# Kernel optimization log

Hardware: AMD Instinct MI355X
Metric: run time of the kernel (lower is better)

## Reference

```python
import jax, jax.numpy as jnp
import numpy as np

N_NODES = 50000
N_EDGES = 800000
IN_FEATS = 256
HIDDEN = 128
OUT_FEATS = 64


def setup_inputs() -> dict:
    key = jax.random.key(0)
    k1, k2, k3, k4, k5 = jax.random.split(key, 5)
    x = jax.random.normal(k1, (N_NODES, IN_FEATS), dtype=jnp.float32)
    src = jax.random.randint(k2, (N_EDGES,), 0, N_NODES, dtype=jnp.int64)
    dst = jax.random.randint(k3, (N_EDGES,), 0, N_NODES, dtype=jnp.int64)
    # Glorot-ish init for linear weights (DGL GraphConv uses xavier_uniform)
    W1 = jax.random.normal(k4, (IN_FEATS, HIDDEN), dtype=jnp.float32) / np.sqrt(IN_FEATS)
    W2 = jax.random.normal(k5, (HIDDEN, OUT_FEATS), dtype=jnp.float32) / np.sqrt(HIDDEN)
    b1 = jnp.zeros((HIDDEN,), dtype=jnp.float32)
    b2 = jnp.zeros((OUT_FEATS,), dtype=jnp.float32)
    return {"x": x, "src": src, "dst": dst, "W1": W1, "b1": b1, "W2": W2, "b2": b2}


def _norms(src, dst, n_nodes):
    ones = jnp.ones(src.shape[0], dtype=jnp.float32)
    deg_out = jax.ops.segment_sum(ones, src, num_segments=n_nodes)
    deg_in = jax.ops.segment_sum(ones, dst, num_segments=n_nodes)
    # DGL clamps zero degrees to 1 to avoid inf
    norm_src = jnp.power(jnp.clip(deg_out, 1.0, None), -0.5)  # [N]
    norm_dst = jnp.power(jnp.clip(deg_in, 1.0, None), -0.5)   # [N]
    return norm_src, norm_dst


def _gcn_layer(h, W, b, src, dst, norm_src, norm_dst, n_nodes):
    # norm='both': D_dst^{-1/2} A D_src^{-1/2} (h W) + b
    # multiply by W first (in_feats >= out_feats -> cheaper aggregation)
    m = (h * norm_src[:, None]) @ W            # [N, out]
    agg = jax.ops.segment_sum(m[src], dst, num_segments=n_nodes)  # [N, out]
    return agg * norm_dst[:, None] + b


def reference(x, src, dst, W1, b1, W2, b2):
    n = x.shape[0]
    norm_src, norm_dst = _norms(src, dst, n)
    h = _gcn_layer(x, W1, b1, src, dst, norm_src, norm_dst, n)
    h = jax.nn.relu(h)
    h = _gcn_layer(h, W2, b2, src, dst, norm_src, norm_dst, n)
    return h
```

## Files before the change

kernel.cpp:

```cpp
#include <hip/hip_runtime.h>

#define N_NODES 50000
#define N_EDGES 800000
#define IN_FEATS 256
#define HIDDEN 128
#define OUT_FEATS 64

#define NB 16384
#define NRANGE 4
#define NBT (NRANGE * NB)
#define NCHUNK 64
#define EPC 12500

typedef _Float16 f16;
typedef _Float16 f16x8 __attribute__((ext_vector_type(8)));
typedef float f32x4 __attribute__((ext_vector_type(4)));

__global__ __launch_bounds__(256) void hist_kernel(
    const int* __restrict__ src, const int* __restrict__ dst,
    unsigned* __restrict__ hist_src, unsigned* __restrict__ hist_dst,
    const float* __restrict__ W1, const float* __restrict__ W2,
    f16* __restrict__ W1T, f16* __restrict__ W2T) {
  __shared__ unsigned ls[NB / 2];
  __shared__ unsigned ld2[NB / 2];
  const int r = blockIdx.x % NRANGE;
  const int c = blockIdx.x / NRANGE;
  const int lo = r * NB;
  for (int i = threadIdx.x; i < NB / 2; i += 256) {
    ls[i] = 0;
    ld2[i] = 0;
  }
  __syncthreads();
  const int4* s4 = (const int4*)(src + c * EPC);
  const int4* d4 = (const int4*)(dst + c * EPC);
  for (int i = threadIdx.x; i < EPC / 4; i += 256) {
    int4 s = s4[i];
    int4 d = d4[i];
    unsigned b;
    b = (unsigned)(s.x - lo); if (b < NB) atomicAdd(&ls[b >> 1], 1u << ((b & 1) << 4));
    b = (unsigned)(s.y - lo); if (b < NB) atomicAdd(&ls[b >> 1], 1u << ((b & 1) << 4));
    b = (unsigned)(s.z - lo); if (b < NB) atomicAdd(&ls[b >> 1], 1u << ((b & 1) << 4));
    b = (unsigned)(s.w - lo); if (b < NB) atomicAdd(&ls[b >> 1], 1u << ((b & 1) << 4));
    b = (unsigned)(d.x - lo); if (b < NB) atomicAdd(&ld2[b >> 1], 1u << ((b & 1) << 4));
    b = (unsigned)(d.y - lo); if (b < NB) atomicAdd(&ld2[b >> 1], 1u << ((b & 1) << 4));
    b = (unsigned)(d.z - lo); if (b < NB) atomicAdd(&ld2[b >> 1], 1u << ((b & 1) << 4));
    b = (unsigned)(d.w - lo); if (b < NB) atomicAdd(&ld2[b >> 1], 1u << ((b & 1) << 4));
  }
  __syncthreads();
  unsigned* hs = hist_src + ((long)c * NBT + lo) / 2;
  unsigned* hd = hist_dst + ((long)c * NBT + lo) / 2;
  for (int i = threadIdx.x; i < NB / 2; i += 256) {
    hs[i] = ls[i];
    hd[i] = ld2[i];
  }
  if (blockIdx.x < 160) {
    int i = blockIdx.x * 256 + threadIdx.x;
    if (i < 128 * 256) {
      int n = i >> 8, k = i & 255;
      W1T[i] = (f16)W1[k * 128 + n];
    } else {
      int j = i - 128 * 256;
      int n = j >> 7, k = j & 127;
      W2T[j] = (f16)W2[k * 64 + n];
    }
  }
}

__global__ __launch_bounds__(256) void reduce_kernel(
    const unsigned* __restrict__ hist_src, unsigned* __restrict__ hist_dst,
    int* __restrict__ deg_in, float* __restrict__ norm_src,
    float* __restrict__ norm_dst, int* __restrict__ partial) {
  const unsigned short* hs = (const unsigned short*)hist_src;
  unsigned short* hd = (unsigned short*)hist_dst;
  int n = blockIdx.x * 256 + threadIdx.x;
  int run = 0;
  if (n < N_NODES) {
    int so = 0;
#pragma unroll 8
    for (int c = 0; c < NCHUNK; ++c) so += hs[(long)c * NBT + n];
    norm_src[n] = rsqrtf((float)max(so, 1));
#pragma unroll 8
    for (int c = 0; c < NCHUNK; ++c) {
      int t = hd[(long)c * NBT + n];
      hd[(long)c * NBT + n] = (unsigned short)run;
      run += t;
    }
    deg_in[n] = run;
    norm_dst[n] = rsqrtf((float)max(run, 1));
  }
  __shared__ int sd[256];
  sd[threadIdx.x] = run;
  __syncthreads();
  for (int s = 128; s > 0; s >>= 1) {
    if (threadIdx.x < s) sd[threadIdx.x] += sd[threadIdx.x + s];
    __syncthreads();
  }
  if (threadIdx.x == 0) partial[blockIdx.x] = sd[0];
}

__global__ __launch_bounds__(256) void scan3(const int* __restrict__ deg,
                                             const int* __restrict__ partial,
                                             int* __restrict__ rowptr) {
  __shared__ int sd[256];
  __shared__ int sp[256];
  const int w = blockIdx.x;
  int pv = (threadIdx.x < 196) ? partial[threadIdx.x] : 0;
  sp[threadIdx.x] = pv;
  __syncthreads();
  for (int off = 1; off < 256; off <<= 1) {
    int t = sp[threadIdx.x] +
            ((threadIdx.x >= off) ? sp[threadIdx.x - off] : 0);
    __syncthreads();
    sp[threadIdx.x] = t;
    __syncthreads();
  }
  const int base = (w == 0) ? 0 : sp[w - 1];
  int i = w * 256 + threadIdx.x;
  int v = (i < N_NODES) ? deg[i] : 0;
  sd[threadIdx.x] = v;
  __syncthreads();
  for (int off = 1; off < 256; off <<= 1) {
    int t = sd[threadIdx.x] +
            ((threadIdx.x >= off) ? sd[threadIdx.x - off] : 0);
    __syncthreads();
    sd[threadIdx.x] = t;
    __syncthreads();
  }
  if (i < N_NODES) rowptr[i] = base + sd[threadIdx.x] - v;
  if (w == 0 && threadIdx.x == 0) rowptr[N_NODES] = N_EDGES;
}

__global__ __launch_bounds__(256) void fill_csr(
    const int* __restrict__ src, const int* __restrict__ dst,
    const int* __restrict__ rowptr, const unsigned* __restrict__ pref32,
    int* __restrict__ col) {
  __shared__ int cur[NB];
  const unsigned short* pref = (const unsigned short*)pref32;
  const int r = blockIdx.x % NRANGE;
  const int c = blockIdx.x / NRANGE;
  const int lo = r * NB;
  for (int i = threadIdx.x; i < NB; i += 256) {
    int n = lo + i;
    cur[i] = (n < N_NODES) ? rowptr[n] + pref[(long)c * NBT + n] : 0;
  }
  __syncthreads();
  const int4* s4 = (const int4*)(src + c * EPC);
  const int4* d4 = (const int4*)(dst + c * EPC);
  for (int i = threadIdx.x; i < EPC / 4; i += 256) {
    int4 s = s4[i];
    int4 d = d4[i];
    unsigned b;
    b = (unsigned)(d.x - lo);
    if (b < NB) col[atomicAdd(&cur[b], 1)] = s.x;
    b = (unsigned)(d.y - lo);
    if (b < NB) col[atomicAdd(&cur[b], 1)] = s.y;
    b = (unsigned)(d.z - lo);
    if (b < NB) col[atomicAdd(&cur[b], 1)] = s.z;
    b = (unsigned)(d.w - lo);
    if (b < NB) col[atomicAdd(&cur[b], 1)] = s.w;
  }
}

template <int K, int NC, int TN, bool FP32IN>
__global__ __launch_bounds__(256) void gemm_mfma(
    const void* __restrict__ Xv, const f16* __restrict__ WT,
    const float* __restrict__ ns, f16* __restrict__ Mout) {
  constexpr int KI = K / 32;
  constexpr int COLBLK = NC / (TN * 16);
  constexpr int KP = K + 8;
  __shared__ f16 Bs[TN * 16 * KP];

  const int cb = blockIdx.x % COLBLK;
  const int rb = blockIdx.x / COLBLK;
  const int col0 = cb * TN * 16;
  const int wave = threadIdx.x >> 6;
  const int lane = threadIdx.x & 63;
  const int m = lane & 15;
  const int q = lane >> 4;
  const int row0 = rb * 64 + wave * 16;

  for (int idx = threadIdx.x; idx < TN * 16 * (K / 8); idx += 256) {
    int n = idx / (K / 8);
    int kk = idx % (K / 8);
    *(f16x8*)(Bs + n * KP + kk * 8) =
        *(const f16x8*)(WT + (long)(col0 + n) * K + kk * 8);
  }
  __syncthreads();

  const int ra = min(row0 + m, N_NODES - 1);
  const float s = FP32IN ? ns[ra] : 0.f;

  f32x4 acc[TN];
#pragma unroll
  for (int t = 0; t < TN; ++t) acc[t] = (f32x4){0.f, 0.f, 0.f, 0.f};

#pragma unroll
  for (int ki = 0; ki < KI; ++ki) {
    const int kb = ki * 32 + q * 8;
    f16x8 a;
    if (FP32IN) {
      const float* X = (const float*)Xv;
      const float* p = X + (long)ra * K + kb;
      float4 u0 = *(const float4*)p;
      float4 u1 = *(const float4*)(p + 4);
      a[0] = (f16)(u0.x * s); a[1] = (f16)(u0.y * s);
      a[2] = (f16)(u0.z * s); a[3] = (f16)(u0.w * s);
      a[4] = (f16)(u1.x * s); a[5] = (f16)(u1.y * s);
      a[6] = (f16)(u1.z * s); a[7] = (f16)(u1.w * s);
    } else {
      const f16* X = (const f16*)Xv;
      a = *(const f16x8*)(X + (long)ra * K + kb);
    }
#pragma unroll
    for (int t = 0; t < TN; ++t) {
      f16x8 b = *(const f16x8*)(Bs + (t * 16 + m) * KP + kb);
      acc[t] = __builtin_amdgcn_mfma_f32_16x16x32_f16(a, b, acc[t], 0, 0, 0);
    }
  }

#pragma unroll
  for (int r = 0; r < 4; ++r) {
    int row = row0 + q * 4 + r;
    if (row < N_NODES) {
#pragma unroll
      for (int t = 0; t < TN; ++t)
        Mout[(long)row * NC + col0 + t * 16 + m] = (f16)acc[t][r];
    }
  }
}

__global__ __launch_bounds__(256) void gather1_kernel(
    const f16* __restrict__ M, const int* __restrict__ rowptr,
    const int* __restrict__ col, const float* __restrict__ nd,
    const float* __restrict__ ns, const float* __restrict__ b,
    f16* __restrict__ out) {
  constexpr int LPR = 16;
  constexpr int EPW = 64 / LPR;
  const int wave = threadIdx.x >> 6;
  const int lane = threadIdx.x & 63;
  const int eg = lane / LPR;
  const int t = lane % LPR;
  const int n = blockIdx.x * 4 + wave;
  if (n >= N_NODES) return;
  const int beg = rowptr[n];
  const int end = rowptr[n + 1];

  float acc[8];
#pragma unroll
  for (int j = 0; j < 8; ++j) acc[j] = 0.f;

  int i = beg + eg;
  for (; i + EPW < end; i += 2 * EPW) {
    int s0 = col[i];
    int s1 = col[i + EPW];
    f16x8 v0 = *(const f16x8*)(M + (long)s0 * HIDDEN + t * 8);
    f16x8 v1 = *(const f16x8*)(M + (long)s1 * HIDDEN + t * 8);
#pragma unroll
    for (int j = 0; j < 8; ++j) acc[j] += (float)v0[j] + (float)v1[j];
  }
  if (i < end) {
    int s0 = col[i];
    f16x8 v0 = *(const f16x8*)(M + (long)s0 * HIDDEN + t * 8);
#pragma unroll
    for (int j = 0; j < 8; ++j) acc[j] += (float)v0[j];
  }

#pragma unroll
  for (int m2 = LPR; m2 < 64; m2 <<= 1)
#pragma unroll
    for (int j = 0; j < 8; ++j) acc[j] += __shfl_xor(acc[j], m2, 64);

  if (eg == 0) {
    float s = nd[n];
    float sn = ns[n];
    float4 bb0 = *(const float4*)(b + t * 8);
    float4 bb1 = *(const float4*)(b + t * 8 + 4);
    f16x8 o;
    o[0] = (f16)(fmaxf(acc[0] * s + bb0.x, 0.f) * sn);
    o[1] = (f16)(fmaxf(acc[1] * s + bb0.y, 0.f) * sn);
    o[2] = (f16)(fmaxf(acc[2] * s + bb0.z, 0.f) * sn);
    o[3] = (f16)(fmaxf(acc[3] * s + bb0.w, 0.f) * sn);
    o[4] = (f16)(fmaxf(acc[4] * s + bb1.x, 0.f) * sn);
    o[5] = (f16)(fmaxf(acc[5] * s + bb1.y, 0.f) * sn);
    o[6] = (f16)(fmaxf(acc[6] * s + bb1.z, 0.f) * sn);
    o[7] = (f16)(fmaxf(acc[7] * s + bb1.w, 0.f) * sn);
    *(f16x8*)(out + (long)n * HIDDEN + t * 8) = o;
  }
}

__global__ __launch_bounds__(256) void gather2_kernel(
    const f16* __restrict__ M, const int* __restrict__ rowptr,
    const int* __restrict__ col, const float* __restrict__ nd,
    const float* __restrict__ b, float* __restrict__ out) {
  constexpr int LPR = 8;
  constexpr int EPW = 64 / LPR;
  const int wave = threadIdx.x >> 6;
  const int lane = threadIdx.x & 63;
  const int eg = lane / LPR;
  const int t = lane % LPR;
  const int n = blockIdx.x * 4 + wave;
  if (n >= N_NODES) return;
  const int beg = rowptr[n];
  const int end = rowptr[n + 1];

  float acc[8];
#pragma unroll
  for (int j = 0; j < 8; ++j) acc[j] = 0.f;

  int i = beg + eg;
  for (; i + EPW < end; i += 2 * EPW) {
    int s0 = col[i];
    int s1 = col[i + EPW];
    f16x8 v0 = *(const f16x8*)(M + (long)s0 * OUT_FEATS + t * 8);
    f16x8 v1 = *(const f16x8*)(M + (long)s1 * OUT_FEATS + t * 8);
#pragma unroll
    for (int j = 0; j < 8; ++j) acc[j] += (float)v0[j] + (float)v1[j];
  }
  if (i < end) {
    int s0 = col[i];
    f16x8 v0 = *(const f16x8*)(M + (long)s0 * OUT_FEATS + t * 8);
#pragma unroll
    for (int j = 0; j < 8; ++j) acc[j] += (float)v0[j];
  }

#pragma unroll
  for (int m2 = LPR; m2 < 64; m2 <<= 1)
#pragma unroll
    for (int j = 0; j < 8; ++j) acc[j] += __shfl_xor(acc[j], m2, 64);

  if (eg == 0) {
    float s = nd[n];
    float4 bb0 = *(const float4*)(b + t * 8);
    float4 bb1 = *(const float4*)(b + t * 8 + 4);
    float4 o0, o1;
    o0.x = acc[0] * s + bb0.x;
    o0.y = acc[1] * s + bb0.y;
    o0.z = acc[2] * s + bb0.z;
    o0.w = acc[3] * s + bb0.w;
    o1.x = acc[4] * s + bb1.x;
    o1.y = acc[5] * s + bb1.y;
    o1.z = acc[6] * s + bb1.z;
    o1.w = acc[7] * s + bb1.w;
    *(float4*)(out + (long)n * OUT_FEATS + t * 8) = o0;
    *(float4*)(out + (long)n * OUT_FEATS + t * 8 + 4) = o1;
  }
}

extern "C" void kernel_launch(void* const* d_in, const int* in_sizes, int n_in,
                              void* d_out, int out_size, void* d_ws,
                              size_t ws_size, hipStream_t stream) {
  const float* x = (const float*)d_in[0];
  const int* src = (const int*)d_in[1];
  const int* dst = (const int*)d_in[2];
  const float* W1 = (const float*)d_in[3];
  const float* b1 = (const float*)d_in[4];
  const float* W2 = (const float*)d_in[5];
  const float* b2 = (const float*)d_in[6];
  float* out = (float*)d_out;

  int* wi = (int*)d_ws;
  int* partial = wi;
  int* rowptr = wi + 256;
  int* deg_in = wi + 50260;
  int* col = wi + 100260;
  float* wf = (float*)d_ws + 900260;
  float* norm_src = wf;
  float* norm_dst = wf + 50000;
  f16* fh = (f16*)(wf + 100000);
  f16* W1T = fh;
  f16* W2T = fh + 128 * 256;
  f16* m1 = fh + 128 * 256 + 64 * 128;
  f16* h1p = m1 + (long)50048 * 128;
  f16* m2 = h1p + (long)50048 * 128;

  unsigned* hist_src = (unsigned*)m1;
  unsigned* hist_dst = hist_src + (long)NCHUNK * NBT / 2;

  const int nb_nodes = (N_NODES + 255) / 256;
  const int rowblk = (N_NODES + 63) / 64;

  hist_kernel<<<NRANGE * NCHUNK, 256, 0, stream>>>(src, dst, hist_src,
                                                   hist_dst, W1, W2, W1T, W2T);
  reduce_kernel<<<nb_nodes, 256, 0, stream>>>(hist_src, hist_dst, deg_in,
                                              norm_src, norm_dst, partial);
  scan3<<<nb_nodes, 256, 0, stream>>>(deg_in, partial, rowptr);
  fill_csr<<<NRANGE * NCHUNK, 256, 0, stream>>>(src, dst, rowptr, hist_dst,
                                                col);

  gemm_mfma<IN_FEATS, HIDDEN, 4, true>
      <<<rowblk * 2, 256, 0, stream>>>(x, W1T, norm_src, m1);
  gather1_kernel<<<(N_NODES + 3) / 4, 256, 0, stream>>>(m1, rowptr, col,
                                                        norm_dst, norm_src, b1,
                                                        h1p);

  gemm_mfma<HIDDEN, OUT_FEATS, 4, false>
      <<<rowblk, 256, 0, stream>>>(h1p, W2T, norm_src, m2);
  gather2_kernel<<<(N_NODES + 3) / 4, 256, 0, stream>>>(m2, rowptr, col,
                                                        norm_dst, b2, out);
}
```

Measured before the change: 236.4 us.

## Fuse first GEMM into histogram kernel and move source norm into gather

The first-layer GEMM (x·W1) is merged into the degree histogram launch as extra blocks. Because the source-degree normalisation is not known yet at that point, the GEMM is done unscaled and the gather multiplies each neighbour row by its norm_src. The histogram tiles shrink (NB 8192, 7 ranges) so the shared-memory footprint fits alongside the GEMM's B tile. Histogram buffers move to the h1p area, and W1 is converted to half precision per block instead of being pre-transposed. This removes one launch and lets the GEMM overlap the histogram, but the gather now does an extra per-edge norm load and multiply.

```diff
diff --git a/kernel.cpp b/kernel.cpp
--- a/kernel.cpp
+++ b/kernel.cpp
@@ -6,62 +6,121 @@
 #define HIDDEN 128
 #define OUT_FEATS 64
 
-#define NB 16384
-#define NRANGE 4
+#define NB 8192
+#define NRANGE 7
 #define NBT (NRANGE * NB)
 #define NCHUNK 64
 #define EPC 12500
+#define HBLK (NRANGE * NCHUNK)
+#define ROWBLK ((N_NODES + 63) / 64)
+#define G1BLK (ROWBLK * 2)
 
 typedef _Float16 f16;
+typedef _Float16 f16x2 __attribute__((ext_vector_type(2)));
 typedef _Float16 f16x8 __attribute__((ext_vector_type(8)));
 typedef float f32x4 __attribute__((ext_vector_type(4)));
 
-__global__ __launch_bounds__(256) void hist_kernel(
+__global__ __launch_bounds__(256) void hist_gemm_kernel(
     const int* __restrict__ src, const int* __restrict__ dst,
     unsigned* __restrict__ hist_src, unsigned* __restrict__ hist_dst,
     const float* __restrict__ W1, const float* __restrict__ W2,
-    f16* __restrict__ W1T, f16* __restrict__ W2T) {
-  __shared__ unsigned ls[NB / 2];
-  __shared__ unsigned ld2[NB / 2];
-  const int r = blockIdx.x % NRANGE;
-  const int c = blockIdx.x / NRANGE;
-  const int lo = r * NB;
-  for (int i = threadIdx.x; i < NB / 2; i += 256) {
-    ls[i] = 0;
-    ld2[i] = 0;
-  }
-  __syncthreads();
-  const int4* s4 = (const int4*)(src + c * EPC);
-  const int4* d4 = (const int4*)(dst + c * EPC);
-  for (int i = threadIdx.x; i < EPC / 4; i += 256) {
-    int4 s = s4[i];
-    int4 d = d4[i];
-    unsigned b;
-    b = (unsigned)(s.x - lo); if (b < NB) atomicAdd(&ls[b >> 1], 1u << ((b & 1) << 4));
-    b = (unsigned)(s.y - lo); if (b < NB) atomicAdd(&ls[b >> 1], 1u << ((b & 1) << 4));
-    b = (unsigned)(s.z - lo); if (b < NB) atomicAdd(&ls[b >> 1], 1u << ((b & 1) << 4));
-    b = (unsigned)(s.w - lo); if (b < NB) atomicAdd(&ls[b >> 1], 1u << ((b & 1) << 4));
-    b = (unsigned)(d.x - lo); if (b < NB) atomicAdd(&ld2[b >> 1], 1u << ((b & 1) << 4));
-    b = (unsigned)(d.y - lo); if (b < NB) atomicAdd(&ld2[b >> 1], 1u << ((b & 1) << 4));
-    b = (unsigned)(d.z - lo); if (b < NB) atomicAdd(&ld2[b >> 1], 1u << ((b & 1) << 4));
-    b = (unsigned)(d.w - lo); if (b < NB) atomicAdd(&ld2[b >> 1], 1u << ((b & 1) << 4));
-  }
-  __syncthreads();
-  unsigned* hs = hist_src + ((long)c * NBT + lo) / 2;
-  unsigned* hd = hist_dst + ((long)c * NBT + lo) / 2;
-  for (int i = threadIdx.x; i < NB / 2; i += 256) {
-    hs[i] = ls[i];
-    hd[i] = ld2[i];
-  }
-  if (blockIdx.x < 160) {
-    int i = blockIdx.x * 256 + threadIdx.x;
-    if (i < 128 * 256) {
-      int n = i >> 8, k = i & 255;
-      W1T[i] = (f16)W1[k * 128 + n];
-    } else {
-      int j = i - 128 * 256;
+    f16* __restrict__ W2T, const float* __restrict__ x,
+    f16* __restrict__ m1) {
+  __shared__ __align__(16) unsigned smem[8448];
+  if (blockIdx.x < HBLK) {
+    unsigned* ls = smem;
+    unsigned* ld2 = smem + NB / 2;
+    const int r = blockIdx.x % NRANGE;
+    const int c = blockIdx.x / NRANGE;
+    const int lo = r * NB;
+    for (int i = threadIdx.x; i < NB / 2; i += 256) {
+      ls[i] = 0;
+      ld2[i] = 0;
+    }
+    __syncthreads();
+    const int4* s4 = (const int4*)(src + c * EPC);
+    const int4* d4 = (const int4*)(dst + c * EPC);
+    for (int i = threadIdx.x; i < EPC / 4; i += 256) {
+      int4 s = s4[i];
+      int4 d = d4[i];
+      unsigned b;
+      b = (unsigned)(s.x - lo); if (b < NB) atomicAdd(&ls[b >> 1], 1u << ((b & 1) << 4));
+      b = (unsigned)(s.y - lo); if (b < NB) atomicAdd(&ls[b >> 1], 1u << ((b & 1) << 4));
+      b = (unsigned)(s.z - lo); if (b < NB) atomicAdd(&ls[b >> 1], 1u << ((b & 1) << 4));
+      b = (unsigned)(s.w - lo); if (b < NB) atomicAdd(&ls[b >> 1], 1u << ((b & 1) << 4));
+      b = (unsigned)(d.x - lo); if (b < NB) atomicAdd(&ld2[b >> 1], 1u << ((b & 1) << 4));
+      b = (unsigned)(d.y - lo); if (b < NB) atomicAdd(&ld2[b >> 1], 1u << ((b & 1) << 4));
+      b = (unsigned)(d.z - lo); if (b < NB) atomicAdd(&ld2[b >> 1], 1u << ((b & 1) << 4));
+      b = (unsigned)(d.w - lo); if (b < NB) atomicAdd(&ld2[b >> 1], 1u << ((b & 1) << 4));
+    }
+    __syncthreads();
+    unsigned* hs = hist_src + ((long)c * NBT + lo) / 2;
+    unsigned* hd = hist_dst + ((long)c * NBT + lo) / 2;
+    for (int i = threadIdx.x; i < NB / 2; i += 256) {
+      hs[i] = ls[i];
+      hd[i] = ld2[i];
+    }
+    if (blockIdx.x < 32) {
+      int j = blockIdx.x * 256 + threadIdx.x;
       int n = j >> 7, k = j & 127;
       W2T[j] = (f16)W2[k * 64 + n];
+    }
+  } else {
+    f16* Bs = (f16*)smem;
+    constexpr int KP = IN_FEATS + 8;
+    const int bid = blockIdx.x - HBLK;
+    const int cb = bid & 1;
+    const int rb = bid >> 1;
+    const int col0 = cb * 64;
+    const int wave = threadIdx.x >> 6;
+    const int lane = threadIdx.x & 63;
+    const int m = lane & 15;
+    const int q = lane >> 4;
+    const int row0 = rb * 64 + wave * 16;
+
+    for (int idx = threadIdx.x; idx < 64 * (IN_FEATS / 2); idx += 256) {
+      int k2 = idx >> 6;
+      int n = idx & 63;
+      float a0 = W1[(2 * k2) * HIDDEN + col0 + n];
+      float a1 = W1[(2 * k2 + 1) * HIDDEN + col0 + n];
+      f16x2 pk;
+      pk[0] = (f16)a0;
+      pk[1] = (f16)a1;
+      *(f16x2*)(Bs + n * KP + 2 * k2) = pk;
+    }
+    __syncthreads();
+
+    const int ra = min(row0 + m, N_NODES - 1);
+    f32x4 acc[4];
+#pragma unroll
+    for (int t = 0; t < 4; ++t) acc[t] = (f32x4){0.f, 0.f, 0.f, 0.f};
+
+#pragma unroll
+    for (int ki = 0; ki < IN_FEATS / 32; ++ki) {
+      const int kb = ki * 32 + q * 8;
+      const float* p = x + (long)ra * IN_FEATS + kb;
+      float4 u0 = *(const float4*)p;
+      float4 u1 = *(const float4*)(p + 4);
+      f16x8 a;
+      a[0] = (f16)u0.x; a[1] = (f16)u0.y;
+      a[2] = (f16)u0.z; a[3] = (f16)u0.w;
+      a[4] = (f16)u1.x; a[5] = (f16)u1.y;
+      a[6] = (f16)u1.z; a[7] = (f16)u1.w;
+#pragma unroll
+      for (int t = 0; t < 4; ++t) {
+        f16x8 bfr = *(const f16x8*)(Bs + (t * 16 + m) * KP + kb);
+        acc[t] = __builtin_amdgcn_mfma_f32_16x16x32_f16(a, bfr, acc[t], 0, 0, 0);
+      }
+    }
+
+#pragma unroll
+    for (int rr = 0; rr < 4; ++rr) {
+      int row = row0 + q * 4 + rr;
+      if (row < N_NODES) {
+#pragma unroll
+        for (int t = 0; t < 4; ++t)
+          m1[(long)row * HIDDEN + col0 + t * 16 + m] = (f16)acc[t][rr];
+      }
     }
   }
 }
@@ -253,16 +312,20 @@
   for (; i + EPW < end; i += 2 * EPW) {
     int s0 = col[i];
     int s1 = col[i + EPW];
+    float n0 = ns[s0];
+    float n1 = ns[s1];
     f16x8 v0 = *(const f16x8*)(M + (long)s0 * HIDDEN + t * 8);
     f16x8 v1 = *(const f16x8*)(M + (long)s1 * HIDDEN + t * 8);
 #pragma unroll
-    for (int j = 0; j < 8; ++j) acc[j] += (float)v0[j] + (float)v1[j];
+    for (int j = 0; j < 8; ++j)
+      acc[j] += n0 * (float)v0[j] + n1 * (float)v1[j];
   }
   if (i < end) {
     int s0 = col[i];
+    float n0 = ns[s0];
     f16x8 v0 = *(const f16x8*)(M + (long)s0 * HIDDEN + t * 8);
 #pragma unroll
-    for (int j = 0; j < 8; ++j) acc[j] += (float)v0[j];
+    for (int j = 0; j < 8; ++j) acc[j] += n0 * (float)v0[j];
   }
 
 #pragma unroll
@@ -367,34 +430,29 @@
   float* norm_src = wf;
   float* norm_dst = wf + 50000;
   f16* fh = (f16*)(wf + 100000);
-  f16* W1T = fh;
-  f16* W2T = fh + 128 * 256;
-  f16* m1 = fh + 128 * 256 + 64 * 128;
+  f16* W2T = fh;
+  f16* m1 = fh + 64 * 128;
   f16* h1p = m1 + (long)50048 * 128;
   f16* m2 = h1p + (long)50048 * 128;
 
-  unsigned* hist_src = (unsigned*)m1;
+  unsigned* hist_src = (unsigned*)h1p;
   unsigned* hist_dst = hist_src + (long)NCHUNK * NBT / 2;
 
   const int nb_nodes = (N_NODES + 255) / 256;
-  const int rowblk = (N_NODES + 63) / 64;
-
-  hist_kernel<<<NRANGE * NCHUNK, 256, 0, stream>>>(src, dst, hist_src,
-                                                   hist_dst, W1, W2, W1T, W2T);
+
+  hist_gemm_kernel<<<HBLK + G1BLK, 256, 0, stream>>>(
+      src, dst, hist_src, hist_dst, W1, W2, W2T, x, m1);
   reduce_kernel<<<nb_nodes, 256, 0, stream>>>(hist_src, hist_dst, deg_in,
                                               norm_src, norm_dst, partial);
   scan3<<<nb_nodes, 256, 0, stream>>>(deg_in, partial, rowptr);
-  fill_csr<<<NRANGE * NCHUNK, 256, 0, stream>>>(src, dst, rowptr, hist_dst,
-                                                col);
-
-  gemm_mfma<IN_FEATS, HIDDEN, 4, true>
-      <<<rowblk * 2, 256, 0, stream>>>(x, W1T, norm_src, m1);
+  fill_csr<<<HBLK, 256, 0, stream>>>(src, dst, rowptr, hist_dst, col);
+
   gather1_kernel<<<(N_NODES + 3) / 4, 256, 0, stream>>>(m1, rowptr, col,
                                                         norm_dst, norm_src, b1,
                                                         h1p);
 
   gemm_mfma<HIDDEN, OUT_FEATS, 4, false>
-      <<<rowblk, 256, 0, stream>>>(h1p, W2T, norm_src, m2);
+      <<<ROWBLK, 256, 0, stream>>>(h1p, W2T, norm_src, m2);
   gather2_kernel<<<(N_NODES + 3) / 4, 256, 0, stream>>>(m2, rowptr, col,
                                                         norm_dst, b2, out);
 }
```

Result: no change. 235.3 us (-0.5%).
